# Optimization experiments

Hardware: AMD Instinct MI355X
Metric: run time of the kernel (lower is better)

The kernel has to match this reference:

```python
import jax, jax.numpy as jnp
import numpy as np

PYRAMID_LEVEL = 3

def _ceil_div(a, b):
    return -(-a // b)

def build_region_masks(H, W, levels=PYRAMID_LEVEL):
    """Binary region-membership matrices per pyramid level (overlap=True).
    Level l has (2**l)**2 overlapping windows; sum-pooling over a window equals
    a matmul with these masks (zero padding contributes nothing)."""
    Ms = []
    for level in range(levels):
        ns = 2 ** level
        h_wid = _ceil_div(2 * H, ns + 1); w_wid = _ceil_div(2 * W, ns + 1)
        h_str = _ceil_div(H, ns + 1);     w_str = _ceil_div(W, ns + 1)
        H_new = h_wid + (ns - 1) * h_str; W_new = w_wid + (ns - 1) * w_str
        pad_top = (H_new - H) // 2; pad_left = (W_new - W) // 2
        M = np.zeros((ns * ns, H, W), np.float32)
        r = 0
        for i in range(ns):
            for j in range(ns):
                h0 = i * h_str - pad_top; w0 = j * w_str - pad_left
                M[r, max(h0, 0):min(h0 + h_wid, H), max(w0, 0):min(w0 + w_wid, W)] = 1.0
                r += 1
        Ms.append(M.reshape(ns * ns, H * W))
    return Ms

def setup_inputs() -> dict:
    key = jax.random.key(0)
    ks = jax.random.split(key, 6)
    N, C, H, W, K, S, L = 32, 128, 48, 48, 64, 4, 3
    return {
        "x": jax.random.normal(ks[0], (N, C, H, W), jnp.float32),
        "centroids": jax.random.uniform(ks[1], (K, C), dtype=jnp.float32),
        "conv_w": jax.random.normal(ks[2], (K, C), jnp.float32) * 0.1,
        "conv_shadow_w": jax.random.normal(ks[3], (K * S, C), jnp.float32) * 0.1,
        "conv_app_w": jax.random.normal(ks[4], (L, K, C), jnp.float32) * 0.1,
        "cluster_weights": jnp.ones((K,), jnp.float32),
    }

def reference(x, centroids, conv_w, conv_shadow_w, conv_app_w, cluster_weights):
    N, C, H, W = x.shape
    K = centroids.shape[0]
    S = conv_shadow_w.shape[0] // K
    L = conv_app_w.shape[0]
    P = H * W
    eps = 1e-12
    # descriptor-wise L2 normalization of input
    x = x / jnp.maximum(jnp.linalg.norm(x, axis=1, keepdims=True), eps)
    xp = x.reshape(N, C, P)
    # 1x1-conv soft assignment (no bias, vladv2=False)
    score = jnp.einsum('kc,ncp->nkp', conv_w, xp)            # [N,K,P]
    a = jax.nn.softmax(score, axis=1)                        # over clusters
    # shadow weighting: each cluster competes with its S shadow clusters
    sh = jnp.einsum('kc,ncp->nkp', conv_shadow_w, xp).reshape(N, K, S, P)
    cat = jnp.concatenate([score[:, :, None, :], sh], axis=2)  # [N,K,1+S,P]
    sal_pix = jax.nn.softmax(cat, axis=2)[:, :, 0, :]          # salient prob
    a = a * sal_pix                                            # [N,K,P]
    # attentional pyramid saliency: per-level 1x1 conv + relu + region sum-pool
    Ms = build_region_masks(H, W, L)
    sal = jnp.concatenate([
        jnp.einsum('nkp,rp->nkr',
                   jax.nn.relu(jnp.einsum('kc,ncp->nkp', conv_app_w[l], xp)),
                   jnp.asarray(Ms[l]))
        for l in range(L)], axis=2)                            # [N,K,R], R=21
    Mall = jnp.asarray(np.concatenate(Ms, axis=0))             # [R,P]
    # fused pyramid aggregation: sum_r sal_r * sumpool_r((x - c_k) * a_k)
    # == contraction with per-pixel weight w = M^T @ sal
    w = jnp.einsum('nkr,rp->nkp', sal, Mall)                   # [N,K,P]
    aw = a * w
    vlad = jnp.einsum('nkp,ncp->nkc', aw, xp) - centroids[None] * aw.sum(-1)[..., None]
    # intra (per-cluster) L2 normalization
    vlad = vlad / jnp.maximum(jnp.linalg.norm(vlad, axis=2, keepdims=True), eps)
    # parametric normalization
    vlad = vlad * cluster_weights[None, :, None]
    v = vlad.reshape(N, K * C)
    return v / jnp.maximum(jnp.linalg.norm(v, axis=1, keepdims=True), eps)
```

## Files before the change

kernel.cpp:

```cpp
#include <hip/hip_runtime.h>
#include <hip/hip_bf16.h>

#define N_ 32
#define C_ 128
#define H_ 48
#define W_ 48
#define P_ (H_*W_)
#define K_ 64
#define S_ 4
#define L_ 3
#define R_ 21
#define NB_ 72
#define M_ 512
#define CH_ 9
#define CHV_ 18

typedef __hip_bfloat16 bf16;
typedef __attribute__((ext_vector_type(8))) short   bf16x8;
typedef __attribute__((ext_vector_type(8))) unsigned short u16x8;
typedef __attribute__((ext_vector_type(4))) unsigned short u16x4;
typedef __attribute__((ext_vector_type(4))) float   f32x4;

__device__ __forceinline__ float b2f(bf16 v){ return __bfloat162float(v); }
__device__ __forceinline__ float u2f(unsigned short u){
  union { unsigned i; float f; } v; v.i = ((unsigned)u) << 16; return v.f;
}
__device__ __forceinline__ unsigned short f2u(float f){
  bf16 h = __float2bfloat16(f);
  return *(unsigned short*)&h;
}

__device__ __forceinline__ int is_f32(const unsigned short* __restrict__ xb){
  int lane = threadIdx.x & 63;
  int w = 0;
  #pragma unroll
  for (int i=0;i<16;++i){
    int e = (xb[lane*16 + i] >> 7) & 0xFF;
    w += (e >= 0x8E) ? 1 : 0;
  }
  unsigned long long b = __ballot(w > 0);
  return __popcll(b) > 32;
}

__device__ __forceinline__ unsigned short region_bit(int r, int h, int w){
  bool m;
  if (r == 0){
    m = true;
  } else if (r < 5){
    int q = r-1, i = q>>1, j = q&1;
    m = (h>=16*i)&&(h<16*i+32)&&(w>=16*j)&&(w<16*j+32);
  } else if (r < 21){
    int q = r-5, i = q>>2, j = q&3;
    m = (h>=10*i-1)&&(h<10*i+19)&&(w>=10*j-1)&&(w<10*j+19);
  } else {
    m = false;
  }
  return m ? (unsigned short)0x3F80 : (unsigned short)0;
}

__global__ __launch_bounds__(256) void k_wall(const void* __restrict__ cvw, const void* __restrict__ csw,
                                              const void* __restrict__ caw, const void* __restrict__ x,
                                              bf16* __restrict__ WallF){
  int f32 = is_f32((const unsigned short*)x);
  int i = blockIdx.x*256 + threadIdx.x;
  int j = i&7, lane = (i>>3)&63, ks = (i>>9)&3, rt = (i>>11)&31;
  int row = rt*16 + (lane&15);
  int c   = ks*32 + ((lane>>4)&3)*8 + j;
  int s = row*C_ + c;
  float v;
  if (s < 8192)       v = f32 ? ((const float*)cvw)[s]        : b2f(((const bf16*)cvw)[s]);
  else if (s < 40960) v = f32 ? ((const float*)csw)[s-8192]   : b2f(((const bf16*)csw)[s-8192]);
  else                v = f32 ? ((const float*)caw)[s-40960]  : b2f(((const bf16*)caw)[s-40960]);
  WallF[i] = __float2bfloat16(v);
}

__global__ __launch_bounds__(256) void k_norm(const void* __restrict__ x,
                                              bf16* __restrict__ xnF,
                                              bf16* __restrict__ xnG){
  __shared__ float sred[2][128];
  __shared__ __align__(16) unsigned short tile[128][136];
  int f32 = is_f32((const unsigned short*)x);
  int bi = blockIdx.x;
  int n = bi / (P_/128), tb = bi % (P_/128);
  int p0 = tb*128;
  int t = threadIdx.x, px = t&127, chh = t>>7, c0 = chh*64;

  float vals[64];
  float ss = 0.f;
  if (f32){
    const float* xb = (const float*)x + ((size_t)n*C_ + c0)*P_ + p0 + px;
    #pragma unroll
    for (int j=0;j<64;++j){ float v = xb[(size_t)j*P_]; vals[j] = v; ss += v*v; }
  } else {
    const unsigned short* xb = (const unsigned short*)x + ((size_t)n*C_ + c0)*P_ + p0 + px;
    #pragma unroll
    for (int j=0;j<64;++j){ float v = u2f(xb[(size_t)j*P_]); vals[j] = v; ss += v*v; }
  }
  sred[chh][px] = ss;
  __syncthreads();
  float invn = 1.f / fmaxf(sqrtf(sred[0][px] + sred[1][px]), 1e-12f);
  unsigned short nv[64];
  #pragma unroll
  for (int j=0;j<64;++j) nv[j] = f2u(vals[j]*invn);

  #pragma unroll
  for (int j=0;j<64;++j) tile[c0+j][px] = nv[j];
  __syncthreads();
  {
    int ch = tb>>1, hb = tb&1;
    size_t gbase = ((size_t)(n*CH_ + ch)*8 + hb*4)*512;
    u16x8* out = (u16x8*)xnG;
    #pragma unroll
    for (int it=0;it<8;++it){
      int o2 = t + it*256;
      int lane = o2&63, half = (o2>>6)&1, wvv = (o2>>7)&3, ksl = (o2>>9)&3;
      int c  = wvv*32 + half*16 + (lane&15);
      int pl = ksl*32 + ((lane>>4)&3)*8;
      out[gbase + o2] = *(const u16x8*)&tile[c][pl];
    }
  }
  __syncthreads();
  #pragma unroll
  for (int j8=0;j8<8;++j8)
    *(u16x8*)&tile[px][c0 + j8*8] = *(const u16x8*)&nv[j8*8];
  __syncthreads();
  {
    size_t fbase = (size_t)(n*NB_ + tb*4)*512;
    u16x8* out = (u16x8*)xnF;
    #pragma unroll
    for (int it=0;it<8;++it){
      int o = t + it*256;
      int lane = o&63, half = (o>>6)&1, ks = (o>>7)&3, pbl = (o>>9)&3;
      int pxr = pbl*32 + half*16 + (lane&15);
      int cc  = ks*32 + ((lane>>4)&3)*8;
      out[fbase + o] = *(const u16x8*)&tile[pxr][cc];
    }
  }
}

__global__ __launch_bounds__(512, 4) void k_gemm(const bf16* __restrict__ WallF,
                                                 const bf16* __restrict__ xnF,
                                                 unsigned short* __restrict__ a,
                                                 float* __restrict__ salPart){
  __shared__ __align__(16) unsigned short ldsU[320][40];
  __shared__ __align__(16) unsigned short appS[192][40];
  int n = blockIdx.y, pb = blockIdx.x;
  int p0 = pb*32;
  int t = threadIdx.x, w = t>>6, l = t&63;
  int mrow = l&15, quad = l>>4;

  const bf16* Af = WallF + ((size_t)(w*4)*4)*512 + l*8;
  const bf16* Bf = xnF + (size_t)(n*NB_ + pb)*4096 + l*8;

  f32x4 acc[4][2];
  #pragma unroll
  for (int rtl=0;rtl<4;++rtl){ acc[rtl][0] = (f32x4){0,0,0,0}; acc[rtl][1] = (f32x4){0,0,0,0}; }

  #pragma unroll
  for (int ks=0;ks<4;++ks){
    bf16x8 b0 = *(const bf16x8*)(Bf + (ks*2+0)*512);
    bf16x8 b1 = *(const bf16x8*)(Bf + (ks*2+1)*512);
    #pragma unroll
    for (int rtl=0;rtl<4;++rtl){
      bf16x8 af = *(const bf16x8*)(Af + (rtl*4+ks)*512);
      acc[rtl][0] = __builtin_amdgcn_mfma_f32_16x16x32_bf16(af, b0, acc[rtl][0], 0,0,0);
      acc[rtl][1] = __builtin_amdgcn_mfma_f32_16x16x32_bf16(af, b1, acc[rtl][1], 0,0,0);
    }
  }

  #pragma unroll
  for (int rtl=0;rtl<4;++rtl){
    int row0 = w*64 + rtl*16;
    if (row0 < 64){
      #pragma unroll
      for (int ct=0;ct<2;++ct)
        #pragma unroll
        for (int r=0;r<4;++r)
          ldsU[row0 + quad*4 + r][ct*16 + mrow] = f2u(acc[rtl][ct][r]);
    } else if (row0 < 320){
      #pragma unroll
      for (int ct=0;ct<2;++ct)
        #pragma unroll
        for (int r=0;r<4;++r){
          int sr = row0 + quad*4 + r - 64;
          ldsU[64 + (sr&3)*64 + (sr>>2)][ct*16 + mrow] = f2u(acc[rtl][ct][r]);
        }
    } else {
      int ar0 = row0 - 320 + quad*4;
      #pragma unroll
      for (int ct=0;ct<2;++ct)
        #pragma unroll
        for (int r=0;r<4;++r)
          appS[ar0 + r][ct*16 + mrow] = f2u(fmaxf(acc[rtl][ct][r], 0.f));
    }
  }
  __syncthreads();

  {
    u16x4 s4  = *(const u16x4*)&ldsU[l      ][w*4];
    u16x4 h0v = *(const u16x4*)&ldsU[64  + l][w*4];
    u16x4 h1v = *(const u16x4*)&ldsU[128 + l][w*4];
    u16x4 h2v = *(const u16x4*)&ldsU[192 + l][w*4];
    u16x4 h3v = *(const u16x4*)&ldsU[256 + l][w*4];
    float ez[4], Zr[4];
    #pragma unroll
    for (int j=0;j<4;++j){ ez[j] = __expf(u2f((unsigned short)s4[j])); Zr[j] = ez[j]; }
    #pragma unroll
    for (int st=1; st<64; st<<=1){
      #pragma unroll
      for (int j=0;j<4;++j) Zr[j] += __shfl_xor(Zr[j], st);
    }
    size_t tile = (size_t)n*NB_ + pb;
    #pragma unroll
    for (int j=0;j<4;++j){
      float e0 = ez[j];
      float den = e0 + __expf(u2f((unsigned short)h0v[j]))
                     + __expf(u2f((unsigned short)h1v[j]))
                     + __expf(u2f((unsigned short)h2v[j]))
                     + __expf(u2f((unsigned short)h3v[j]));
      a[tile*2048 + (size_t)(w*4+j)*64 + l] = f2u(__fdividef(e0*e0, Zr[j]*den));
    }
  }

  bf16x8 bm0;
  #pragma unroll
  for (int j=0;j<8;++j){
    int p = p0 + quad*8 + j;
    int h = p/48, wc = p - h*48;
    bm0[j] = (short)region_bit(mrow, h, wc);
  }
  size_t tile = (size_t)n*NB_ + pb;
  float* sp = salPart + tile*(K_*R_);
  if (w < 4){
    #pragma unroll
    for (int i=0;i<2;++i){
      int rt = w*2 + i;
      bf16x8 af = *(const bf16x8*)&appS[rt*16 + mrow][quad*8];
      f32x4 r0 = (f32x4){0,0,0,0};
      r0 = __builtin_amdgcn_mfma_f32_16x16x32_bf16(af, bm0, r0, 0,0,0);
      int kb = rt*16 + quad*4;
      if (rt < 4){
        if (mrow == 0){
          #pragma unroll
          for (int r=0;r<4;++r) sp[(size_t)(kb+r)*R_] = r0[r];
        }
      } else {
        if (mrow >= 1 && mrow <= 4){
          #pragma unroll
          for (int r=0;r<4;++r) sp[(size_t)(kb+r-64)*R_ + mrow] = r0[r];
        }
      }
    }
  } else {
    int rt = 8 + (w-4);
    bf16x8 bm1;
    #pragma unroll
    for (int j=0;j<8;++j){
      int p = p0 + quad*8 + j;
      int h = p/48, wc = p - h*48;
      bm1[j] = (short)region_bit(16 + mrow, h, wc);
    }
    bf16x8 af = *(const bf16x8*)&appS[rt*16 + mrow][quad*8];
    f32x4 r0 = (f32x4){0,0,0,0}, r1 = (f32x4){0,0,0,0};
    r0 = __builtin_amdgcn_mfma_f32_16x16x32_bf16(af, bm0, r0, 0,0,0);
    r1 = __builtin_amdgcn_mfma_f32_16x16x32_bf16(af, bm1, r1, 0,0,0);
    int kb = rt*16 + quad*4;
    if (mrow >= 5){
      #pragma unroll
      for (int r=0;r<4;++r) sp[(size_t)(kb+r-128)*R_ + mrow] = r0[r];
    } else {
      #pragma unroll
      for (int r=0;r<4;++r) sp[(size_t)(kb+r-128)*R_ + 16 + mrow] = r1[r];
    }
  }
}

__global__ __launch_bounds__(256) void k_salred(const float* __restrict__ salPart,
                                                float* __restrict__ sal){
  int tid = blockIdx.x*256 + threadIdx.x;
  if (tid >= N_*K_*R_) return;
  int n = tid / (K_*R_), i = tid - n*(K_*R_);
  const float* sp = salPart + (size_t)n*NB_*(K_*R_) + i;
  float s = 0.f;
  #pragma unroll 8
  for (int b=0;b<NB_;++b) s += sp[(size_t)b*(K_*R_)];
  sal[tid] = s;
}

__global__ __launch_bounds__(512) void k_vlad(const bf16* __restrict__ xnG,
                                              const unsigned short* __restrict__ a,
                                              const float* __restrict__ sal,
                                              float* __restrict__ vladPart,
                                              float* __restrict__ sumawPart){
  __shared__ float s_sal[K_][R_];
  __shared__ __align__(16) unsigned short awL[4][K_][40];
  __shared__ float s_part[4][K_];
  int c2 = blockIdx.x, n = blockIdx.y, t = threadIdx.x;
  int p0 = c2*128;
  for (int i=t;i<K_*R_;i+=512) ((float*)s_sal)[i] = sal[(size_t)n*K_*R_ + i];
  __syncthreads();

  {
    int pxl = t & 127, kq = t>>7;
    int pbl = pxl>>5, px = pxl&31;
    int p = p0 + pxl;
    int h = p/48, wc = p - h*48;
    bool h1[2], w1[2], h2[4], w2[4];
    #pragma unroll
    for (int i=0;i<2;++i){ h1[i] = (h>=16*i)&&(h<16*i+32); w1[i] = (wc>=16*i)&&(wc<16*i+32); }
    #pragma unroll
    for (int i=0;i<4;++i){ h2[i] = (h>=10*i-1)&&(h<10*i+19); w2[i] = (wc>=10*i-1)&&(wc<10*i+19); }
    const unsigned short* at = a + ((size_t)((n*NB_ + c2*4 + pbl)*32 + px))*K_ + kq*16;
    u16x8 av[2];
    av[0] = *(const u16x8*)at;
    av[1] = *(const u16x8*)(at + 8);
    #pragma unroll
    for (int kk=0;kk<16;++kk){
      int k = kq*16 + kk;
      float w = s_sal[k][0];
      #pragma unroll
      for (int i=0;i<2;++i) if (h1[i])
        #pragma unroll
        for (int j=0;j<2;++j) if (w1[j]) w += s_sal[k][1+2*i+j];
      #pragma unroll
      for (int i=0;i<4;++i) if (h2[i])
        #pragma unroll
        for (int j=0;j<4;++j) if (w2[j]) w += s_sal[k][5+4*i+j];
      awL[pbl][k][px] = f2u(u2f(av[kk>>3][kk&7]) * w);
    }
  }
  __syncthreads();
  if (t < 256){
    int k = t&63, qr = t>>6;
    float s = 0.f;
    #pragma unroll 8
    for (int j=0;j<32;++j) s += u2f(awL[qr][k][j]);
    s_part[qr][k] = s;
  }
  __syncthreads();

  int wave = t>>6, l = t&63, mrow = l&15, quad = l>>4;
  int wvc = wave&3, mh = wave>>2;
  f32x4 acc[2][2];
  #pragma unroll
  for (int mtl=0;mtl<2;++mtl){ acc[mtl][0] = (f32x4){0,0,0,0}; acc[mtl][1] = (f32x4){0,0,0,0}; }
  const bf16* Gf = xnG + (size_t)(n*CH_ + (c2>>1))*32768 + l*8;
  int ksbase = (c2&1)*4;
  #pragma unroll
  for (int ksl=0;ksl<4;++ksl){
    int ks = ksbase + ksl;
    bf16x8 b0 = *(const bf16x8*)(Gf + ((ks*4+wvc)*2+0)*512);
    bf16x8 b1 = *(const bf16x8*)(Gf + ((ks*4+wvc)*2+1)*512);
    #pragma unroll
    for (int mtl=0;mtl<2;++mtl){
      bf16x8 af = *(const bf16x8*)((const bf16*)&awL[ksl][(mh*2+mtl)*16 + mrow][quad*8]);
      acc[mtl][0] = __builtin_amdgcn_mfma_f32_16x16x32_bf16(af, b0, acc[mtl][0], 0,0,0);
      acc[mtl][1] = __builtin_amdgcn_mfma_f32_16x16x32_bf16(af, b1, acc[mtl][1], 0,0,0);
    }
  }
  float* vp = vladPart + ((size_t)(n*CHV_ + c2))*(K_*C_);
  #pragma unroll
  for (int mtl=0;mtl<2;++mtl){
    #pragma unroll
    for (int ct=0;ct<2;++ct){
      int c = wvc*32 + ct*16 + mrow;
      #pragma unroll
      for (int r=0;r<4;++r){
        int k = (mh*2+mtl)*16 + quad*4 + r;
        vp[k*C_ + c] = acc[mtl][ct][r];
      }
    }
  }
  if (t < K_){
    float s = s_part[0][t] + s_part[1][t] + s_part[2][t] + s_part[3][t];
    sumawPart[((size_t)n*CHV_ + c2)*K_ + t] = s;
  }
}

__global__ __launch_bounds__(256) void k_vred(const float* __restrict__ vladPart,
                                              const float* __restrict__ sumawPart,
                                              const void* __restrict__ cen,
                                              const void* __restrict__ x,
                                              float* __restrict__ vlad){
  int f32 = is_f32((const unsigned short*)x);
  int tid = blockIdx.x*256 + threadIdx.x;
  int n = tid >> 13;
  int i = tid & 8191;
  int k = i >> 7;
  const float* vp = vladPart + (size_t)n*CHV_*(K_*C_) + i;
  float s = 0.f;
  #pragma unroll
  for (int ch=0;ch<CHV_;++ch) s += vp[(size_t)ch*(K_*C_)];
  float sw = 0.f;
  #pragma unroll
  for (int ch=0;ch<CHV_;++ch) sw += sumawPart[((size_t)n*CHV_ + ch)*K_ + k];
  float cv = f32 ? ((const float*)cen)[i] : b2f(((const bf16*)cen)[i]);
  vlad[tid] = s - cv*sw;
}

__global__ __launch_bounds__(256) void k_final(const float* __restrict__ vlad,
                                               const void* __restrict__ clw,
                                               const void* __restrict__ x,
                                               void* __restrict__ out){
  __shared__ float s_v[K_*C_];
  __shared__ float s_ssk[K_];
  __shared__ float s_scale[K_];
  __shared__ float s_gs;
  int n = blockIdx.x, t = threadIdx.x;
  int f32 = is_f32((const unsigned short*)x);
  const float* vp = vlad + (size_t)n*K_*C_;
  for (int i=t;i<K_*C_;i+=256) s_v[i] = vp[i];
  __syncthreads();
  int k = t >> 2, q = t & 3;
  float ss = 0.f;
  for (int mm=0;mm<32;++mm){ float v = s_v[k*C_ + q + 4*mm]; ss += v*v; }
  ss += __shfl_down(ss, 2);
  ss += __shfl_down(ss, 1);
  if (q == 0) s_ssk[k] = ss;
  __syncthreads();
  if (t < K_){
    float cw = f32 ? ((const float*)clw)[t] : b2f(((const bf16*)clw)[t]);
    s_scale[t] = cw / fmaxf(sqrtf(s_ssk[t]), 1e-12f);
  }
  __syncthreads();
  if (t == 0){
    float gss = 0.f;
    for (int kk=0;kk<K_;++kk) gss += s_ssk[kk]*s_scale[kk]*s_scale[kk];
    s_gs = 1.f / fmaxf(sqrtf(gss), 1e-12f);
  }
  __syncthreads();
  float gsc = s_gs;
  if (f32){
    float* op = (float*)out + (size_t)n*K_*C_;
    for (int i=t;i<K_*C_;i+=256) op[i] = s_v[i]*s_scale[i>>7]*gsc;
  } else {
    bf16* op = (bf16*)out + (size_t)n*K_*C_;
    for (int i=t;i<K_*C_;i+=256) op[i] = __float2bfloat16(s_v[i]*s_scale[i>>7]*gsc);
  }
}

extern "C" void kernel_launch(void* const* d_in, const int* in_sizes, int n_in,
                              void* d_out, int out_size, void* d_ws, size_t ws_size,
                              hipStream_t stream){
  const void* x   = d_in[0];
  const void* cen = d_in[1];
  const void* cvw = d_in[2];
  const void* csw = d_in[3];
  const void* caw = d_in[4];
  const void* clw = d_in[5];

  char* ws = (char*)d_ws;
  bf16* WallF = (bf16*)ws;             ws += (size_t)M_*C_*2;
  bf16* xnF   = (bf16*)ws;             ws += (size_t)N_*P_*C_*2;
  bf16* xnG   = (bf16*)ws;             ws += (size_t)N_*C_*P_*2;
  char* aBuf  = ws;                    ws += (size_t)N_*K_*P_*2;
  unsigned short* a = (unsigned short*)aBuf;
  float* vlad = (float*)aBuf;
  float* sal  = (float*)ws;            ws += (size_t)N_*K_*R_*4;
  char* un = ws;
  float* salPart   = (float*)un;
  float* sumawPart = (float*)un;
  ws += (size_t)N_*NB_*K_*R_*4;
  float* vladPart = (float*)xnF;

  k_wall  <<<dim3(M_*C_/256),       256, 0, stream>>>(cvw, csw, caw, x, WallF);
  k_norm  <<<dim3(N_*P_/128),       256, 0, stream>>>(x, xnF, xnG);
  k_gemm  <<<dim3(NB_, N_),         512, 0, stream>>>(WallF, xnF, a, salPart);
  k_salred<<<dim3((N_*K_*R_+255)/256), 256, 0, stream>>>(salPart, sal);
  k_vlad  <<<dim3(CHV_, N_),        512, 0, stream>>>(xnG, a, sal, vladPart, sumawPart);
  k_vred  <<<dim3(N_*K_*C_/256),    256, 0, stream>>>(vladPart, sumawPart, cen, x, vlad);
  k_final <<<dim3(N_),              256, 0, stream>>>(vlad, clw, x, d_out);
}
```

Measured before the change: 153.5 us.

## Fuse weight-pack and normalize kernels, halve tiles for more blocks in norm and vlad

```diff
diff --git a/kernel.cpp b/kernel.cpp
--- a/kernel.cpp
+++ b/kernel.cpp
@@ -13,7 +13,8 @@
 #define NB_ 72
 #define M_ 512
 #define CH_ 9
-#define CHV_ 18
+#define CHV_ 36
+#define NBK_ 1152
 
 typedef __hip_bfloat16 bf16;
 typedef __attribute__((ext_vector_type(8))) short   bf16x8;
@@ -58,82 +59,107 @@
   return m ? (unsigned short)0x3F80 : (unsigned short)0;
 }
 
-__global__ __launch_bounds__(256) void k_wall(const void* __restrict__ cvw, const void* __restrict__ csw,
-                                              const void* __restrict__ caw, const void* __restrict__ x,
-                                              bf16* __restrict__ WallF){
+__global__ __launch_bounds__(256, 6) void k_prep(const void* __restrict__ cvw, const void* __restrict__ csw,
+                                                 const void* __restrict__ caw, const void* __restrict__ x,
+                                                 bf16* __restrict__ WallF, bf16* __restrict__ xnF,
+                                                 bf16* __restrict__ xnG){
+  int bid = blockIdx.x, t = threadIdx.x;
   int f32 = is_f32((const unsigned short*)x);
-  int i = blockIdx.x*256 + threadIdx.x;
-  int j = i&7, lane = (i>>3)&63, ks = (i>>9)&3, rt = (i>>11)&31;
-  int row = rt*16 + (lane&15);
-  int c   = ks*32 + ((lane>>4)&3)*8 + j;
-  int s = row*C_ + c;
-  float v;
-  if (s < 8192)       v = f32 ? ((const float*)cvw)[s]        : b2f(((const bf16*)cvw)[s]);
-  else if (s < 40960) v = f32 ? ((const float*)csw)[s-8192]   : b2f(((const bf16*)csw)[s-8192]);
-  else                v = f32 ? ((const float*)caw)[s-40960]  : b2f(((const bf16*)caw)[s-40960]);
-  WallF[i] = __float2bfloat16(v);
-}
-
-__global__ __launch_bounds__(256) void k_norm(const void* __restrict__ x,
-                                              bf16* __restrict__ xnF,
-                                              bf16* __restrict__ xnG){
-  __shared__ float sred[2][128];
-  __shared__ __align__(16) unsigned short tile[128][136];
-  int f32 = is_f32((const unsigned short*)x);
-  int bi = blockIdx.x;
-  int n = bi / (P_/128), tb = bi % (P_/128);
-  int p0 = tb*128;
-  int t = threadIdx.x, px = t&127, chh = t>>7, c0 = chh*64;
-
-  float vals[64];
+  if (bid >= NBK_){
+    int i = (bid - NBK_)*256 + t;
+    int j = i&7, lane = (i>>3)&63, ks = (i>>9)&3, rt = (i>>11)&31;
+    int row = rt*16 + (lane&15);
+    int c   = ks*32 + ((lane>>4)&3)*8 + j;
+    int s = row*C_ + c;
+    float v;
+    if (s < 8192)       v = f32 ? ((const float*)cvw)[s]        : b2f(((const bf16*)cvw)[s]);
+    else if (s < 40960) v = f32 ? ((const float*)csw)[s-8192]   : b2f(((const bf16*)csw)[s-8192]);
+    else                v = f32 ? ((const float*)caw)[s-40960]  : b2f(((const bf16*)caw)[s-40960]);
+    WallF[i] = __float2bfloat16(v);
+    return;
+  }
+
+  __shared__ float sred[4][64];
+  __shared__ __align__(16) unsigned short tile[128][72];
+  int n = bid / (P_/64), tb = bid % (P_/64);
+  int p0 = tb*64;
+  int px = t&63, chh = t>>6, c0 = chh*32;
+
+  size_t off = ((size_t)n*C_ + c0)*P_ + p0 + px;
   float ss = 0.f;
   if (f32){
-    const float* xb = (const float*)x + ((size_t)n*C_ + c0)*P_ + p0 + px;
-    #pragma unroll
-    for (int j=0;j<64;++j){ float v = xb[(size_t)j*P_]; vals[j] = v; ss += v*v; }
+    const volatile float* xb = (const volatile float*)x + off;
+    #pragma unroll
+    for (int j8=0;j8<4;++j8){
+      float tv[8];
+      #pragma unroll
+      for (int j=0;j<8;++j) tv[j] = xb[(size_t)(j8*8+j)*P_];
+      #pragma unroll
+      for (int j=0;j<8;++j) ss += tv[j]*tv[j];
+    }
   } else {
-    const unsigned short* xb = (const unsigned short*)x + ((size_t)n*C_ + c0)*P_ + p0 + px;
-    #pragma unroll
-    for (int j=0;j<64;++j){ float v = u2f(xb[(size_t)j*P_]); vals[j] = v; ss += v*v; }
+    const volatile unsigned short* xb = (const volatile unsigned short*)x + off;
+    #pragma unroll
+    for (int j8=0;j8<4;++j8){
+      float tv[8];
+      #pragma unroll
+      for (int j=0;j<8;++j) tv[j] = u2f(xb[(size_t)(j8*8+j)*P_]);
+      #pragma unroll
+      for (int j=0;j<8;++j) ss += tv[j]*tv[j];
+    }
   }
   sred[chh][px] = ss;
   __syncthreads();
-  float invn = 1.f / fmaxf(sqrtf(sred[0][px] + sred[1][px]), 1e-12f);
-  unsigned short nv[64];
-  #pragma unroll
-  for (int j=0;j<64;++j) nv[j] = f2u(vals[j]*invn);
-
-  #pragma unroll
-  for (int j=0;j<64;++j) tile[c0+j][px] = nv[j];
-  __syncthreads();
+  float invn = 1.f / fmaxf(sqrtf(sred[0][px] + sred[1][px] + sred[2][px] + sred[3][px]), 1e-12f);
+
+  if (f32){
+    const float* xb = (const float*)x + off;
+    #pragma unroll
+    for (int j8=0;j8<4;++j8){
+      float tv[8];
+      #pragma unroll
+      for (int j=0;j<8;++j) tv[j] = xb[(size_t)(j8*8+j)*P_];
+      #pragma unroll
+      for (int j=0;j<8;++j) tile[c0 + j8*8 + j][px] = f2u(tv[j]*invn);
+    }
+  } else {
+    const unsigned short* xb = (const unsigned short*)x + off;
+    #pragma unroll
+    for (int j8=0;j8<4;++j8){
+      float tv[8];
+      #pragma unroll
+      for (int j=0;j<8;++j) tv[j] = u2f(xb[(size_t)(j8*8+j)*P_]);
+      #pragma unroll
+      for (int j=0;j<8;++j) tile[c0 + j8*8 + j][px] = f2u(tv[j]*invn);
+    }
+  }
+  __syncthreads();
+
   {
-    int ch = tb>>1, hb = tb&1;
-    size_t gbase = ((size_t)(n*CH_ + ch)*8 + hb*4)*512;
+    size_t gbase = (size_t)(n*CH_ + (tb>>2))*4096 + (size_t)(tb&3)*1024;
     u16x8* out = (u16x8*)xnG;
     #pragma unroll
-    for (int it=0;it<8;++it){
+    for (int it=0;it<4;++it){
       int o2 = t + it*256;
-      int lane = o2&63, half = (o2>>6)&1, wvv = (o2>>7)&3, ksl = (o2>>9)&3;
-      int c  = wvv*32 + half*16 + (lane&15);
-      int pl = ksl*32 + ((lane>>4)&3)*8;
-      out[gbase + o2] = *(const u16x8*)&tile[c][pl];
-    }
-  }
-  __syncthreads();
-  #pragma unroll
-  for (int j8=0;j8<8;++j8)
-    *(u16x8*)&tile[px][c0 + j8*8] = *(const u16x8*)&nv[j8*8];
-  __syncthreads();
+      int lane = o2&63, half = (o2>>6)&1, wvv = (o2>>7)&3, kslL = (o2>>9)&1;
+      int c   = wvv*32 + half*16 + (lane&15);
+      int plL = kslL*32 + ((lane>>4)&3)*8;
+      out[gbase + o2] = *(const u16x8*)&tile[c][plL];
+    }
+  }
   {
-    size_t fbase = (size_t)(n*NB_ + tb*4)*512;
+    size_t fbase = (size_t)(n*NB_ + tb*2)*512;
     u16x8* out = (u16x8*)xnF;
     #pragma unroll
-    for (int it=0;it<8;++it){
+    for (int it=0;it<4;++it){
       int o = t + it*256;
-      int lane = o&63, half = (o>>6)&1, ks = (o>>7)&3, pbl = (o>>9)&3;
-      int pxr = pbl*32 + half*16 + (lane&15);
+      int lane = o&63, half = (o>>6)&1, ks = (o>>7)&3, pblL = (o>>9)&1;
+      int pxr = pblL*32 + half*16 + (lane&15);
       int cc  = ks*32 + ((lane>>4)&3)*8;
-      out[fbase + o] = *(const u16x8*)&tile[pxr][cc];
+      u16x8 pk;
+      #pragma unroll
+      for (int j=0;j<8;++j) pk[j] = tile[cc+j][pxr];
+      out[fbase + o] = pk;
     }
   }
 }
@@ -293,15 +319,15 @@
                                               float* __restrict__ vladPart,
                                               float* __restrict__ sumawPart){
   __shared__ float s_sal[K_][R_];
-  __shared__ __align__(16) unsigned short awL[4][K_][40];
-  __shared__ float s_part[4][K_];
+  __shared__ __align__(16) unsigned short awL[2][K_][40];
+  __shared__ float s_part[2][K_];
   int c2 = blockIdx.x, n = blockIdx.y, t = threadIdx.x;
-  int p0 = c2*128;
+  int p0 = c2*64;
   for (int i=t;i<K_*R_;i+=512) ((float*)s_sal)[i] = sal[(size_t)n*K_*R_ + i];
   __syncthreads();
 
   {
-    int pxl = t & 127, kq = t>>7;
+    int pxl = t & 63, kq = t>>6;
     int pbl = pxl>>5, px = pxl&31;
     int p = p0 + pxl;
     int h = p/48, wc = p - h*48;
@@ -310,13 +336,11 @@
     for (int i=0;i<2;++i){ h1[i] = (h>=16*i)&&(h<16*i+32); w1[i] = (wc>=16*i)&&(wc<16*i+32); }
     #pragma unroll
     for (int i=0;i<4;++i){ h2[i] = (h>=10*i-1)&&(h<10*i+19); w2[i] = (wc>=10*i-1)&&(wc<10*i+19); }
-    const unsigned short* at = a + ((size_t)((n*NB_ + c2*4 + pbl)*32 + px))*K_ + kq*16;
-    u16x8 av[2];
-    av[0] = *(const u16x8*)at;
-    av[1] = *(const u16x8*)(at + 8);
-    #pragma unroll
-    for (int kk=0;kk<16;++kk){
-      int k = kq*16 + kk;
+    const unsigned short* at = a + ((size_t)((n*NB_ + c2*2 + pbl)*32 + px))*K_ + kq*8;
+    u16x8 av = *(const u16x8*)at;
+    #pragma unroll
+    for (int kk=0;kk<8;++kk){
+      int k = kq*8 + kk;
       float w = s_sal[k][0];
       #pragma unroll
       for (int i=0;i<2;++i) if (h1[i])
@@ -326,11 +350,11 @@
       for (int i=0;i<4;++i) if (h2[i])
         #pragma unroll
         for (int j=0;j<4;++j) if (w2[j]) w += s_sal[k][5+4*i+j];
-      awL[pbl][k][px] = f2u(u2f(av[kk>>3][kk&7]) * w);
-    }
-  }
-  __syncthreads();
-  if (t < 256){
+      awL[pbl][k][px] = f2u(u2f(av[kk]) * w);
+    }
+  }
+  __syncthreads();
+  if (t < 128){
     int k = t&63, qr = t>>6;
     float s = 0.f;
     #pragma unroll 8
@@ -344,10 +368,10 @@
   f32x4 acc[2][2];
   #pragma unroll
   for (int mtl=0;mtl<2;++mtl){ acc[mtl][0] = (f32x4){0,0,0,0}; acc[mtl][1] = (f32x4){0,0,0,0}; }
-  const bf16* Gf = xnG + (size_t)(n*CH_ + (c2>>1))*32768 + l*8;
-  int ksbase = (c2&1)*4;
-  #pragma unroll
-  for (int ksl=0;ksl<4;++ksl){
+  const bf16* Gf = xnG + (size_t)(n*CH_ + (c2>>2))*32768 + l*8;
+  int ksbase = (c2&3)*2;
+  #pragma unroll
+  for (int ksl=0;ksl<2;++ksl){
     int ks = ksbase + ksl;
     bf16x8 b0 = *(const bf16x8*)(Gf + ((ks*4+wvc)*2+0)*512);
     bf16x8 b1 = *(const bf16x8*)(Gf + ((ks*4+wvc)*2+1)*512);
@@ -372,8 +396,7 @@
     }
   }
   if (t < K_){
-    float s = s_part[0][t] + s_part[1][t] + s_part[2][t] + s_part[3][t];
-    sumawPart[((size_t)n*CHV_ + c2)*K_ + t] = s;
+    sumawPart[((size_t)n*CHV_ + c2)*K_ + t] = s_part[0][t] + s_part[1][t];
   }
 }
 
@@ -389,10 +412,10 @@
   int k = i >> 7;
   const float* vp = vladPart + (size_t)n*CHV_*(K_*C_) + i;
   float s = 0.f;
-  #pragma unroll
+  #pragma unroll 6
   for (int ch=0;ch<CHV_;++ch) s += vp[(size_t)ch*(K_*C_)];
   float sw = 0.f;
-  #pragma unroll
+  #pragma unroll 6
   for (int ch=0;ch<CHV_;++ch) sw += sumawPart[((size_t)n*CHV_ + ch)*K_ + k];
   float cv = f32 ? ((const float*)cen)[i] : b2f(((const bf16*)cen)[i]);
   vlad[tid] = s - cv*sw;
@@ -453,21 +476,19 @@
   bf16* WallF = (bf16*)ws;             ws += (size_t)M_*C_*2;
   bf16* xnF   = (bf16*)ws;             ws += (size_t)N_*P_*C_*2;
   bf16* xnG   = (bf16*)ws;             ws += (size_t)N_*C_*P_*2;
-  char* aBuf  = ws;                    ws += (size_t)N_*K_*P_*2;
-  unsigned short* a = (unsigned short*)aBuf;
-  float* vlad = (float*)aBuf;
+  unsigned short* a = (unsigned short*)ws;  ws += (size_t)N_*K_*P_*2;
+  float* vlad = (float*)a;
   float* sal  = (float*)ws;            ws += (size_t)N_*K_*R_*4;
   char* un = ws;
   float* salPart   = (float*)un;
   float* sumawPart = (float*)un;
   ws += (size_t)N_*NB_*K_*R_*4;
-  float* vladPart = (float*)xnF;
-
-  k_wall  <<<dim3(M_*C_/256),       256, 0, stream>>>(cvw, csw, caw, x, WallF);
-  k_norm  <<<dim3(N_*P_/128),       256, 0, stream>>>(x, xnF, xnG);
-  k_gemm  <<<dim3(NB_, N_),         512, 0, stream>>>(WallF, xnF, a, salPart);
+  float* vladPart = (float*)ws;        ws += (size_t)N_*CHV_*K_*C_*4;
+
+  k_prep  <<<dim3(NBK_ + M_*C_/256), 256, 0, stream>>>(cvw, csw, caw, x, WallF, xnF, xnG);
+  k_gemm  <<<dim3(NB_, N_),          512, 0, stream>>>(WallF, xnF, a, salPart);
   k_salred<<<dim3((N_*K_*R_+255)/256), 256, 0, stream>>>(salPart, sal);
-  k_vlad  <<<dim3(CHV_, N_),        512, 0, stream>>>(xnG, a, sal, vladPart, sumawPart);
-  k_vred  <<<dim3(N_*K_*C_/256),    256, 0, stream>>>(vladPart, sumawPart, cen, x, vlad);
-  k_final <<<dim3(N_),              256, 0, stream>>>(vlad, clw, x, d_out);
-}
+  k_vlad  <<<dim3(CHV_, N_),         512, 0, stream>>>(xnG, a, sal, vladPart, sumawPart);
+  k_vred  <<<dim3(N_*K_*C_/256),     256, 0, stream>>>(vladPart, sumawPart, cen, x, vlad);
+  k_final <<<dim3(N_),               256, 0, stream>>>(vlad, clw, x, d_out);
+}
```

New measurement: 169.8 us. +10.7%, slower.
